# Optimization experiments

Hardware: AMD Instinct MI355X
Metric: run time of the kernel (lower is better)

Reference implementation:

```python
import jax, jax.numpy as jnp
import numpy as np

N_QUBITS = 4  # kernel_size**2 with kernel_size=2 (circuit hardwires wires 0..3)
DEPTH = 1


def _ry(t):
    # RY(t) = [[cos(t/2), -sin(t/2)], [sin(t/2), cos(t/2)]]; t scalar or [B]
    c = jnp.cos(t / 2).astype(jnp.complex64)
    s = jnp.sin(t / 2).astype(jnp.complex64)
    return jnp.stack([jnp.stack([c, -s], -1), jnp.stack([s, c], -1)], -2)


def _rx(t):
    # RX(t) = [[cos(t/2), -i sin(t/2)], [-i sin(t/2), cos(t/2)]]
    c = jnp.cos(t / 2).astype(jnp.complex64)
    js = (-1j) * jnp.sin(t / 2).astype(jnp.complex64)
    return jnp.stack([jnp.stack([c, js], -1), jnp.stack([js, c], -1)], -2)


def _apply1(state, gate, wire):
    # state: [B,2,2,2,2]; gate: [2,2] (shared) or [B,2,2] (per-sample)
    s = jnp.moveaxis(state, 1 + wire, 1)
    if gate.ndim == 2:
        s = jnp.einsum('ij,bj...->bi...', gate, s)
    else:
        s = jnp.einsum('bij,bj...->bi...', gate, s)
    return jnp.moveaxis(s, 1, 1 + wire)


def _cnot(state, c, t):
    s = jnp.moveaxis(state, (1 + c, 1 + t), (1, 2))
    s = s.at[:, 1].set(s[:, 1, ::-1])
    return jnp.moveaxis(s, (1, 2), (1 + c, 1 + t))


def _circuit(x, weights):
    B = x.shape[0]
    state = jnp.zeros((B, 2, 2, 2, 2), jnp.complex64).at[:, 0, 0, 0, 0].set(1.0)
    # AngleEmbedding: RY(pi * x_q) on each wire q (per-sample angles)
    angles = x * jnp.pi
    for q in range(N_QUBITS):
        state = _apply1(state, _ry(angles[:, q]), q)
    w = weights.reshape(DEPTH, N_QUBITS)
    for l in range(DEPTH):
        state = _apply1(state, _rx(w[l, 0]), 0)
        state = _apply1(state, _rx(w[l, 1]), 1)
        state = _cnot(state, 2, 3)
        state = _cnot(state, 0, 2)
        state = _cnot(state, 0, 3)
        state = _apply1(state, _ry(w[l, 2]), 0)
        state = _apply1(state, _ry(w[l, 3]), 3)
    probs = state.real ** 2 + state.imag ** 2  # [B,2,2,2,2] float32
    # <Z_q> = P(bit_q = 0) - P(bit_q = 1)
    evs = []
    for q in range(N_QUBITS):
        p = jnp.moveaxis(probs, 1 + q, 1)
        evs.append((p[:, 0] - p[:, 1]).sum(axis=(1, 2, 3)))
    return jnp.stack(evs, -1)  # [B, 4]


def setup_inputs() -> dict:
    key = jax.random.key(0)
    k1, _ = jax.random.split(key)
    B = 262144
    x = jax.random.uniform(k1, (B, N_QUBITS), dtype=jnp.float32)
    # forward() in the original uses torch.zeros for the circuit weights
    weights = jnp.zeros((DEPTH * N_QUBITS,), dtype=jnp.float32)
    return {"x": x, "weights": weights}


def reference(x, weights):
    return _circuit(x, weights)
```

## Files before the change

### kernel.cpp

```cpp
#include <hip/hip_runtime.h>
#include <math.h>


__global__ __launch_bounds__(256) void quanv_kernel(
    const float* __restrict__ x,
    const float* __restrict__ w,
    float* __restrict__ out,
    int B)
{
    int b = blockIdx.x * blockDim.x + threadIdx.x;
    if (b >= B) return;

    float4 xv = reinterpret_cast<const float4*>(x)[b];

    const float HALF_PI = 1.57079632679489662f;
    float c0, s0, c1, s1, c2, s2, c3, s3;
    __sincosf(xv.x * HALF_PI, &s0, &c0);
    __sincosf(xv.y * HALF_PI, &s1, &c1);
    __sincosf(xv.z * HALF_PI, &s2, &c2);
    __sincosf(xv.w * HALF_PI, &s3, &c3);

    float cw0, sw0, cw1, sw1, cw2, sw2, cw3, sw3;
    __sincosf(w[0] * 0.5f, &sw0, &cw0);
    __sincosf(w[1] * 0.5f, &sw1, &cw1);
    __sincosf(w[2] * 0.5f, &sw2, &cw2);
    __sincosf(w[3] * 0.5f, &sw3, &cw3);

    float f0[2] = {c0, s0}, f1[2] = {c1, s1}, f2[2] = {c2, s2}, f3[2] = {c3, s3};
    float re[16], im[16];
#pragma unroll
    for (int i = 0; i < 16; ++i) {
        re[i] = f0[(i >> 3) & 1] * f1[(i >> 2) & 1] * f2[(i >> 1) & 1] * f3[i & 1];
        im[i] = 0.0f;
    }

#pragma unroll
    for (int i = 0; i < 8; ++i) {
        int i0 = i, i1 = i | 8;
        float r0 = re[i0], m0 = im[i0], r1 = re[i1], m1 = im[i1];
        re[i0] = cw0 * r0 + sw0 * m1;  im[i0] = cw0 * m0 - sw0 * r1;
        re[i1] = sw0 * m0 + cw0 * r1;  im[i1] = -sw0 * r0 + cw0 * m1;
    }
#pragma unroll
    for (int i = 0; i < 16; ++i) {
        if (i & 4) continue;
        int i0 = i, i1 = i | 4;
        float r0 = re[i0], m0 = im[i0], r1 = re[i1], m1 = im[i1];
        re[i0] = cw1 * r0 + sw1 * m1;  im[i0] = cw1 * m0 - sw1 * r1;
        re[i1] = sw1 * m0 + cw1 * r1;  im[i1] = -sw1 * r0 + cw1 * m1;
    }

#pragma unroll
    for (int i = 0; i < 16; ++i) {
        if ((i & 2) && !(i & 1)) {
            float tr = re[i], tm = im[i];
            re[i] = re[i | 1]; im[i] = im[i | 1];
            re[i | 1] = tr;    im[i | 1] = tm;
        }
    }
#pragma unroll
    for (int i = 0; i < 16; ++i) {
        if ((i & 8) && !(i & 2)) {
            float tr = re[i], tm = im[i];
            re[i] = re[i | 2]; im[i] = im[i | 2];
            re[i | 2] = tr;    im[i | 2] = tm;
        }
    }
#pragma unroll
    for (int i = 0; i < 16; ++i) {
        if ((i & 8) && !(i & 1)) {
            float tr = re[i], tm = im[i];
            re[i] = re[i | 1]; im[i] = im[i | 1];
            re[i | 1] = tr;    im[i | 1] = tm;
        }
    }

#pragma unroll
    for (int i = 0; i < 8; ++i) {
        int i0 = i, i1 = i | 8;
        float r0 = re[i0], m0 = im[i0], r1 = re[i1], m1 = im[i1];
        re[i0] = cw2 * r0 - sw2 * r1;  im[i0] = cw2 * m0 - sw2 * m1;
        re[i1] = sw2 * r0 + cw2 * r1;  im[i1] = sw2 * m0 + cw2 * m1;
    }
#pragma unroll
    for (int i = 0; i < 16; ++i) {
        if (i & 1) continue;
        int i0 = i, i1 = i | 1;
        float r0 = re[i0], m0 = im[i0], r1 = re[i1], m1 = im[i1];
        re[i0] = cw3 * r0 - sw3 * r1;  im[i0] = cw3 * m0 - sw3 * m1;
        re[i1] = sw3 * r0 + cw3 * r1;  im[i1] = sw3 * m0 + cw3 * m1;
    }

    float ev0 = 0.f, ev1 = 0.f, ev2 = 0.f, ev3 = 0.f;
#pragma unroll
    for (int i = 0; i < 16; ++i) {
        float p = re[i] * re[i] + im[i] * im[i];
        ev0 += (i & 8) ? -p : p;
        ev1 += (i & 4) ? -p : p;
        ev2 += (i & 2) ? -p : p;
        ev3 += (i & 1) ? -p : p;
    }

    reinterpret_cast<float4*>(out)[b] = make_float4(ev0, ev1, ev2, ev3);
}

extern "C" void kernel_launch(void* const* d_in, const int* in_sizes, int n_in,
                              void* d_out, int out_size, void* d_ws, size_t ws_size,
                              hipStream_t stream) {
    const float* x = (const float*)d_in[0];
    const float* w = (const float*)d_in[1];
    float* out = (float*)d_out;
    int B = in_sizes[0] / 4;
    int block = 256;
    int grid = (B + block - 1) / block;
    quanv_kernel<<<grid, block, 0, stream>>>(x, w, out, B);
}
```

Measured before the change: 59.06 us.

## Factor qubit 1 out of the circuit and compute expectations analytically

Replaces the 16-amplitude statevector simulation with a factored form. Qubit 1 never interacts with the other qubits, so its probabilities are computed separately, and the CNOTs are folded into index permutations of a 3-qubit product. This cuts the per-thread ALU and register work. The kernel is likely memory-bound (16 bytes in and 16 out per sample), so the arithmetic savings may not show in the total time.

```diff
diff --git a/kernel.cpp b/kernel.cpp
--- a/kernel.cpp
+++ b/kernel.cpp
@@ -26,80 +26,59 @@
     __sincosf(w[2] * 0.5f, &sw2, &cw2);
     __sincosf(w[3] * 0.5f, &sw3, &cw3);
 
-    float f0[2] = {c0, s0}, f1[2] = {c1, s1}, f2[2] = {c2, s2}, f3[2] = {c3, s3};
-    float re[16], im[16];
+    float a0r = cw0 * c0, a0i = -sw0 * s0;
+    float a1r = cw0 * s0, a1i = -sw0 * c0;
+    float b0r = cw1 * c1, b0i = -sw1 * s1;
+    float b1r = cw1 * s1, b1i = -sw1 * c1;
+    float pb0 = b0r * b0r + b0i * b0i;
+    float pb1 = b1r * b1r + b1i * b1i;
+
+    float g00 = c2 * c3, g01 = c2 * s3, g10 = s2 * s3, g11 = s2 * c3;
+    float ur[4] = {a0r * g00, a0r * g01, a0r * g10, a0r * g11};
+    float ui[4] = {a0i * g00, a0i * g01, a0i * g10, a0i * g11};
+    float vr[4] = {a1r * g11, a1r * g10, a1r * g01, a1r * g00};
+    float vi[4] = {a1i * g11, a1i * g10, a1i * g01, a1i * g00};
+
+    float A0r[4], A0i[4], A1r[4], A1i[4];
 #pragma unroll
-    for (int i = 0; i < 16; ++i) {
-        re[i] = f0[(i >> 3) & 1] * f1[(i >> 2) & 1] * f2[(i >> 1) & 1] * f3[i & 1];
-        im[i] = 0.0f;
+    for (int k = 0; k < 4; ++k) {
+        A0r[k] = cw2 * ur[k] - sw2 * vr[k];
+        A0i[k] = cw2 * ui[k] - sw2 * vi[k];
+        A1r[k] = sw2 * ur[k] + cw2 * vr[k];
+        A1i[k] = sw2 * ui[k] + cw2 * vi[k];
     }
 
+    float q[2][4];
 #pragma unroll
-    for (int i = 0; i < 8; ++i) {
-        int i0 = i, i1 = i | 8;
-        float r0 = re[i0], m0 = im[i0], r1 = re[i1], m1 = im[i1];
-        re[i0] = cw0 * r0 + sw0 * m1;  im[i0] = cw0 * m0 - sw0 * r1;
-        re[i1] = sw0 * m0 + cw0 * r1;  im[i1] = -sw0 * r0 + cw0 * m1;
-    }
-#pragma unroll
-    for (int i = 0; i < 16; ++i) {
-        if (i & 4) continue;
-        int i0 = i, i1 = i | 4;
-        float r0 = re[i0], m0 = im[i0], r1 = re[i1], m1 = im[i1];
-        re[i0] = cw1 * r0 + sw1 * m1;  im[i0] = cw1 * m0 - sw1 * r1;
-        re[i1] = sw1 * m0 + cw1 * r1;  im[i1] = -sw1 * r0 + cw1 * m1;
+    for (int i2 = 0; i2 < 2; ++i2) {
+        int k0 = i2 * 2, k1 = k0 + 1;
+        float C0r = cw3 * A0r[k0] - sw3 * A0r[k1];
+        float C0i = cw3 * A0i[k0] - sw3 * A0i[k1];
+        float C1r = sw3 * A0r[k0] + cw3 * A0r[k1];
+        float C1i = sw3 * A0i[k0] + cw3 * A0i[k1];
+        q[0][k0] = C0r * C0r + C0i * C0i;
+        q[0][k1] = C1r * C1r + C1i * C1i;
+        float D0r = cw3 * A1r[k0] - sw3 * A1r[k1];
+        float D0i = cw3 * A1i[k0] - sw3 * A1i[k1];
+        float D1r = sw3 * A1r[k0] + cw3 * A1r[k1];
+        float D1i = sw3 * A1i[k0] + cw3 * A1i[k1];
+        q[1][k0] = D0r * D0r + D0i * D0i;
+        q[1][k1] = D1r * D1r + D1i * D1i;
     }
 
-#pragma unroll
-    for (int i = 0; i < 16; ++i) {
-        if ((i & 2) && !(i & 1)) {
-            float tr = re[i], tm = im[i];
-            re[i] = re[i | 1]; im[i] = im[i | 1];
-            re[i | 1] = tr;    im[i | 1] = tm;
-        }
-    }
-#pragma unroll
-    for (int i = 0; i < 16; ++i) {
-        if ((i & 8) && !(i & 2)) {
-            float tr = re[i], tm = im[i];
-            re[i] = re[i | 2]; im[i] = im[i | 2];
-            re[i | 2] = tr;    im[i | 2] = tm;
-        }
-    }
-#pragma unroll
-    for (int i = 0; i < 16; ++i) {
-        if ((i & 8) && !(i & 1)) {
-            float tr = re[i], tm = im[i];
-            re[i] = re[i | 1]; im[i] = im[i | 1];
-            re[i | 1] = tr;    im[i | 1] = tm;
-        }
-    }
+    float s_i0_0 = q[0][0] + q[0][1] + q[0][2] + q[0][3];
+    float s_i0_1 = q[1][0] + q[1][1] + q[1][2] + q[1][3];
+    float S = s_i0_0 + s_i0_1;
+    float z2 = (q[0][0] + q[0][1] + q[1][0] + q[1][1])
+             - (q[0][2] + q[0][3] + q[1][2] + q[1][3]);
+    float z3 = (q[0][0] + q[0][2] + q[1][0] + q[1][2])
+             - (q[0][1] + q[0][3] + q[1][1] + q[1][3]);
+    float pb_sum = pb0 + pb1;
 
-#pragma unroll
-    for (int i = 0; i < 8; ++i) {
-        int i0 = i, i1 = i | 8;
-        float r0 = re[i0], m0 = im[i0], r1 = re[i1], m1 = im[i1];
-        re[i0] = cw2 * r0 - sw2 * r1;  im[i0] = cw2 * m0 - sw2 * m1;
-        re[i1] = sw2 * r0 + cw2 * r1;  im[i1] = sw2 * m0 + cw2 * m1;
-    }
-#pragma unroll
-    for (int i = 0; i < 16; ++i) {
-        if (i & 1) continue;
-        int i0 = i, i1 = i | 1;
-        float r0 = re[i0], m0 = im[i0], r1 = re[i1], m1 = im[i1];
-        re[i0] = cw3 * r0 - sw3 * r1;  im[i0] = cw3 * m0 - sw3 * m1;
-        re[i1] = sw3 * r0 + cw3 * r1;  im[i1] = sw3 * m0 + cw3 * m1;
-    }
-
-    float ev0 = 0.f, ev1 = 0.f, ev2 = 0.f, ev3 = 0.f;
-#pragma unroll
-    for (int i = 0; i < 16; ++i) {
-        float p = re[i] * re[i] + im[i] * im[i];
-        ev0 += (i & 8) ? -p : p;
-        ev1 += (i & 4) ? -p : p;
-        ev2 += (i & 2) ? -p : p;
-        ev3 += (i & 1) ? -p : p;
-    }
+    float ev0 = (s_i0_0 - s_i0_1) * pb_sum;
+    float ev1 = (pb0 - pb1) * S;
+    float ev2 = z2 * pb_sum;
+    float ev3 = z3 * pb_sum;
 
     reinterpret_cast<float4*>(out)[b] = make_float4(ev0, ev1, ev2, ev3);
 }
```

Measured after the change: 57.80 us. 1.02x faster.
